# Kernel optimization log

Measured on AMD Instinct MI355X. Metric: run time of the kernel, lower is better.

## Reference

```python
import jax, jax.numpy as jnp
import numpy as np
from jax import lax

# Model dims (match init_kwargs / Mamba2 defaults)
B = 8; C_IN = 512; C_OUT = 512; H = 32; W = 32; L = H * W
D_STATE = 64; D_CONV = 4; EXPAND = 2; HEADDIM = 64
D_INNER = EXPAND * C_IN            # 1024
NHEADS = D_INNER // HEADDIM        # 16
D_XBC = D_INNER + 2 * D_STATE      # 1152 (ngroups=1)
D_IN_PROJ = 2 * D_INNER + 2 * D_STATE + NHEADS
EPS = 1e-5


def setup_inputs() -> dict:
    key = jax.random.key(0)
    ks = jax.random.split(key, 16)
    x = jax.random.normal(ks[0], (B, C_IN, H, W), jnp.float32)
    ln_w = jnp.ones((C_IN,), jnp.float32)
    ln_b = jnp.zeros((C_IN,), jnp.float32)
    in_proj_w = jax.random.normal(ks[1], (D_IN_PROJ, C_IN), jnp.float32) * 0.02
    conv1d_w = jax.random.normal(ks[2], (D_XBC, D_CONV), jnp.float32) * 0.2
    conv1d_b = jax.random.normal(ks[3], (D_XBC,), jnp.float32) * 0.02
    dt0 = jax.random.uniform(ks[4], (NHEADS,), jnp.float32, 1e-3, 0.1)
    dt_bias = jnp.log(jnp.expm1(dt0))  # inverse softplus init
    A_log = jnp.log(jax.random.uniform(ks[5], (NHEADS,), jnp.float32, 1.0, 16.0))
    D = jax.random.normal(ks[6], (NHEADS,), jnp.float32)
    rms_w = jnp.ones((D_INNER,), jnp.float32)
    out_proj_w = jax.random.normal(ks[7], (C_IN, D_INNER), jnp.float32) * 0.02
    conv2d_w = jax.random.normal(ks[8], (C_OUT, C_IN), jnp.float32) * 0.04
    conv2d_b = jnp.zeros((C_OUT,), jnp.float32)
    bn_g = jnp.ones((C_OUT,), jnp.float32)
    bn_b = jnp.zeros((C_OUT,), jnp.float32)
    bn_mean = jnp.zeros((C_OUT,), jnp.float32)
    bn_var = jnp.ones((C_OUT,), jnp.float32)
    return dict(x=x, ln_w=ln_w, ln_b=ln_b, in_proj_w=in_proj_w, conv1d_w=conv1d_w,
                conv1d_b=conv1d_b, dt_bias=dt_bias, A_log=A_log, D=D, rms_w=rms_w,
                out_proj_w=out_proj_w, conv2d_w=conv2d_w, conv2d_b=conv2d_b,
                bn_g=bn_g, bn_b=bn_b, bn_mean=bn_mean, bn_var=bn_var)


def reference(x, ln_w, ln_b, in_proj_w, conv1d_w, conv1d_b, dt_bias, A_log, D,
              rms_w, out_proj_w, conv2d_w, conv2d_b, bn_g, bn_b, bn_mean, bn_var):
    Bb, C, Hh, Ww = x.shape
    Ltok = Hh * Ww
    # tokens: (B, L, C)
    t = x.reshape(Bb, C, Ltok).transpose(0, 2, 1)
    # LayerNorm over channel dim
    mu = jnp.mean(t, -1, keepdims=True)
    var = jnp.mean(jnp.square(t - mu), -1, keepdims=True)
    xn = (t - mu) * lax.rsqrt(var + EPS) * ln_w + ln_b
    # Mamba2 in_proj -> [z, xBC, dt]
    zxbcdt = jnp.einsum('blc,dc->bld', xn, in_proj_w)
    z = zxbcdt[..., :D_INNER]
    xBC = zxbcdt[..., D_INNER:D_INNER + D_XBC]
    dt = zxbcdt[..., D_INNER + D_XBC:]                       # (B, L, nheads)
    # causal depthwise conv1d + silu
    conv = lax.conv_general_dilated(xBC.transpose(0, 2, 1), conv1d_w[:, None, :],
                                    window_strides=(1,), padding=[(D_CONV - 1, 0)],
                                    feature_group_count=D_XBC)
    xBC = jax.nn.silu(conv.transpose(0, 2, 1) + conv1d_b)
    xh = xBC[..., :D_INNER].reshape(Bb, Ltok, NHEADS, HEADDIM)
    Bm = xBC[..., D_INNER:D_INNER + D_STATE]                 # (B, L, d_state)
    Cm = xBC[..., D_INNER + D_STATE:]
    dt = jax.nn.softplus(dt + dt_bias)
    A = -jnp.exp(A_log)                                      # (nheads,)
    # selective scan (SSD recurrence), state h: (B, nheads, headdim, d_state)
    def step(h, inp):
        xt, dtt, Bt, Ct = inp
        dA = jnp.exp(dtt * A)                                # (B, nheads)
        h = h * dA[..., None, None] + jnp.einsum('bh,bhp,bs->bhps', dtt, xt, Bt)
        y = jnp.einsum('bhps,bs->bhp', h, Ct)
        return h, y
    h0 = jnp.zeros((Bb, NHEADS, HEADDIM, D_STATE), x.dtype)
    xs = (xh.transpose(1, 0, 2, 3), dt.transpose(1, 0, 2),
          Bm.transpose(1, 0, 2), Cm.transpose(1, 0, 2))
    _, ys = lax.scan(step, h0, xs)
    y = ys.transpose(1, 0, 2, 3) + D[None, None, :, None] * xh
    y = y.reshape(Bb, Ltok, D_INNER)
    # gated RMSNorm
    y = y * jax.nn.silu(z)
    y = y * lax.rsqrt(jnp.mean(y * y, -1, keepdims=True) + EPS) * rms_w
    out = jnp.einsum('bld,cd->blc', y, out_proj_w)
    img = out.transpose(0, 2, 1).reshape(Bb, C, Hh, Ww)
    # 1x1 conv + BN (inference) + ReLU
    c = jnp.einsum('bchw,oc->bohw', img, conv2d_w) + conv2d_b[None, :, None, None]
    c = (c - bn_mean[None, :, None, None]) * lax.rsqrt(bn_var + EPS)[None, :, None, None]
    c = c * bn_g[None, :, None, None] + bn_b[None, :, None, None]
    return jax.nn.relu(c)
```

## Files before the change

### kernel.cpp

```cpp
#include <hip/hip_runtime.h>
#include <hip/hip_bf16.h>

#define NB 8
#define LL 1024
#define CIN 512
#define DIN 1024
#define DXBC 1152
#define DPROJ 2192
#define NPADW 2304
#define NHH 16
#define HDD 64
#define DST 64
#define NCHUNK 16
#define QCH 64
#define XBCS 1024
#define CTT 8
#define DTB 16

typedef unsigned short u16;
typedef unsigned int u32;
typedef __bf16 bf16x8 __attribute__((ext_vector_type(8)));
typedef float f32x4 __attribute__((ext_vector_type(4)));
typedef u16 u16x8 __attribute__((ext_vector_type(8)));

__device__ __forceinline__ float bf2f(u16 u) {
    u32 x = ((u32)u) << 16; float f; __builtin_memcpy(&f, &x, 4); return f;
}
__device__ __forceinline__ u16 f2bf(float f) {
    u32 x; __builtin_memcpy(&x, &f, 4);
    u32 r = x + 0x7fff + ((x >> 16) & 1);
    return (u16)(r >> 16);
}

__device__ __forceinline__ void gload16(const u16* g, u16* l) {
    __builtin_amdgcn_global_load_lds((__attribute__((address_space(1))) void*)(g),
                                     (__attribute__((address_space(3))) void*)(l), 16, 0, 0);
}

__device__ __forceinline__ int swz(int row, int cb) {
    return row * 64 + ((cb ^ ((row & 7) << 4)) >> 1);
}

__global__ void f2bf_kernel(const float* __restrict__ s, u16* __restrict__ d, int n) {
    int i = blockIdx.x * 256 + threadIdx.x;
    if (i < n) d[i] = f2bf(s[i]);
}
__global__ void f2bf_pad(const float* __restrict__ s, u16* __restrict__ d, int nsrc, int ndst) {
    int i = blockIdx.x * 256 + threadIdx.x;
    if (i < ndst) d[i] = (i < nsrc) ? f2bf(s[i]) : (u16)0;
}
__global__ __launch_bounds__(256) void woutT_conv(const float* __restrict__ s,
                                                  const float* __restrict__ rw,
                                                  u16* __restrict__ dt) {
    __shared__ float tile[64][65];
    int bc = blockIdx.x & 7, bd = blockIdx.x >> 3;
    int c0 = bc * 64, d0 = bd * 64;
    int t = threadIdx.x;
    int r4 = t >> 6, cc = t & 63;
#pragma unroll
    for (int rr = 0; rr < 16; ++rr) {
        int row = r4 * 16 + rr;
        tile[row][cc] = s[(size_t)(c0 + row) * DIN + d0 + cc];
    }
    __syncthreads();
#pragma unroll
    for (int rr = 0; rr < 16; ++rr) {
        int row = r4 * 16 + rr;
        dt[(size_t)(d0 + row) * CIN + c0 + cc] = f2bf(tile[cc][row] * rw[d0 + row]);
    }
}
__global__ void bn_prep(const float* __restrict__ cb, const float* __restrict__ g,
                        const float* __restrict__ bb, const float* __restrict__ mean,
                        const float* __restrict__ var, float* __restrict__ scale,
                        float* __restrict__ shift) {
    int i = blockIdx.x * 256 + threadIdx.x;
    if (i < CIN) {
        float rs = rsqrtf(var[i] + 1e-5f);
        float sc = g[i] * rs;
        scale[i] = sc;
        shift[i] = (cb[i] - mean[i]) * sc + bb[i];
    }
}

__global__ __launch_bounds__(256) void ln_kernel(const float* __restrict__ x,
                                                 const float* __restrict__ lw,
                                                 const float* __restrict__ lb,
                                                 u16* __restrict__ xn) {
    __shared__ u16 tile[CIN * 33];
    __shared__ float psum[8][32], psq[8][32], muA[32], rsA[32];
    int bid = blockIdx.x;
    int b = bid >> 5, hw0 = (bid & 31) * 32;
    int t = threadIdx.x;
    int hw = t & 31, cg = t >> 5;
    const float* xb = x + (size_t)b * CIN * LL + hw0 + hw;
    float s = 0.f, sq = 0.f;
    for (int r = 0; r < CIN / 8; ++r) {
        int c = r * 8 + cg;
        float v = xb[(size_t)c * LL];
        s += v; sq += v * v;
        tile[c * 33 + hw] = f2bf(v);
    }
    psum[cg][hw] = s; psq[cg][hw] = sq;
    __syncthreads();
    if (t < 32) {
        float ss = 0.f, qq = 0.f;
        for (int g = 0; g < 8; ++g) { ss += psum[g][t]; qq += psq[g][t]; }
        float mu = ss * (1.f / CIN);
        float var = qq * (1.f / CIN) - mu * mu;
        muA[t] = mu; rsA[t] = rsqrtf(var + 1e-5f);
    }
    __syncthreads();
    for (int r = 0; r < 64; ++r) {
        int idx = r * 256 + t;
        int c = idx & (CIN - 1);
        int hh = idx >> 9;
        float v = (bf2f(tile[c * 33 + hh]) - muA[hh]) * rsA[hh] * lw[c] + lb[c];
        xn[((size_t)(b * LL + hw0 + hh)) * CIN + c] = f2bf(v);
    }
}

template <int EPI>
__global__ __launch_bounds__(256) void gemm_bt(const u16* __restrict__ A, const u16* __restrict__ Bw,
                                               void* __restrict__ Cout, int M, int N, int K, int ldc,
                                               int nx,
                                               const float* __restrict__ scale,
                                               const float* __restrict__ shift,
                                               const float* __restrict__ rsc) {
    __shared__ u16 As[2][128 * 64], Bs[2][128 * 64];
    int t = threadIdx.x;
    int lane = t & 63, wave = t >> 6;
    int nblk = gridDim.x;
    int qq = nblk >> 3, rm = nblk & 7;
    int xcd = blockIdx.x & 7, idx = blockIdx.x >> 3;
    int swzb = (xcd < rm ? xcd * (qq + 1) : rm * (qq + 1) + (xcd - rm) * qq) + idx;
    int m0 = (swzb / nx) * 128, n0 = (swzb % nx) * 128;
    int wr = wave >> 1, wc = wave & 1;
    f32x4 acc[4][4];
    for (int m = 0; m < 4; ++m)
        for (int n = 0; n < 4; ++n)
            for (int q = 0; q < 4; ++q) acc[m][n][q] = 0.f;

    const u16* Arow = A + (size_t)m0 * K;
    const u16* Brow = Bw + (size_t)n0 * K;
    int s4 = lane >> 4;
    int rr = lane & 15;

    auto STAGE = [&](int buf, int k0) {
#pragma unroll
        for (int j = 0; j < 4; ++j) {
            int e = j * 256 + t;
            int r = e >> 3, sr = e & 7;
            int src = (sr ^ (r & 7)) * 8;
            gload16(Arow + (size_t)r * K + k0 + src, &As[buf][e * 8]);
            gload16(Brow + (size_t)r * K + k0 + src, &Bs[buf][e * 8]);
        }
    };

    STAGE(0, 0);
    int NK = K >> 6, cur = 0;
    for (int kt = 0; kt < NK; ++kt) {
        if (kt + 1 < NK) {
            STAGE(cur ^ 1, (kt + 1) << 6);
            asm volatile("s_waitcnt vmcnt(8)" ::: "memory");
        } else {
            asm volatile("s_waitcnt vmcnt(0)" ::: "memory");
        }
        __builtin_amdgcn_s_barrier();
        __builtin_amdgcn_sched_barrier(0);
#pragma unroll
        for (int kk = 0; kk < 2; ++kk) {
            bf16x8 af[4], bfr[4];
#pragma unroll
            for (int m = 0; m < 4; ++m) {
                int row = wr * 64 + m * 16 + rr;
                int ss = (kk * 4 + s4) ^ (row & 7);
                af[m] = *(const bf16x8*)&As[cur][row * 64 + ss * 8];
            }
#pragma unroll
            for (int n = 0; n < 4; ++n) {
                int row = wc * 64 + n * 16 + rr;
                int ss = (kk * 4 + s4) ^ (row & 7);
                bfr[n] = *(const bf16x8*)&Bs[cur][row * 64 + ss * 8];
            }
#pragma unroll
            for (int m = 0; m < 4; ++m)
#pragma unroll
                for (int n = 0; n < 4; ++n)
                    acc[m][n] = __builtin_amdgcn_mfma_f32_16x16x32_bf16(af[m], bfr[n], acc[m][n], 0, 0, 0);
        }
        __builtin_amdgcn_s_barrier();
        cur ^= 1;
    }
    int fq = lane >> 4, fr = lane & 15;
#pragma unroll
    for (int m = 0; m < 4; ++m) {
#pragma unroll
        for (int n = 0; n < 4; ++n) {
            int col = n0 + wc * 64 + n * 16 + fr;
#pragma unroll
            for (int q = 0; q < 4; ++q) {
                int row = m0 + wr * 64 + m * 16 + fq * 4 + q;
                float v = acc[m][n][q];
                if (EPI == 0) {
                    ((u16*)Cout)[(size_t)row * ldc + col] = f2bf(v);
                } else {
                    v = v * rsc[col];
                    v = v * scale[row] + shift[row];
                    v = v > 0.f ? v : 0.f;
                    ((float*)Cout)[((size_t)(col >> 10)) * (CIN * LL) + (size_t)row * LL + (col & 1023)] = v;
                }
            }
        }
    }
}

__global__ __launch_bounds__(288) void conv1d_fused(const u16* __restrict__ zx,
                                                    const float* __restrict__ w,
                                                    const float* __restrict__ bias,
                                                    u16* __restrict__ xbc,
                                                    float* __restrict__ Bc, float* __restrict__ Cc) {
    int bid = blockIdx.x;
    int b = bid >> 7;
    int l0 = (bid & 127) * CTT;
    int t = threadIdx.x;
    bool isX = t < 256;
    int ch = isX ? t * 4 : 1024 + (t - 256) * 4;

    float4 wv0 = *(const float4*)&w[(ch + 0) * 4];
    float4 wv1 = *(const float4*)&w[(ch + 1) * 4];
    float4 wv2 = *(const float4*)&w[(ch + 2) * 4];
    float4 wv3 = *(const float4*)&w[(ch + 3) * 4];
    float4 bv = *(const float4*)&bias[ch];

    ushort4 xin[CTT + 3];
    const u16* src = zx + (size_t)(b * LL + l0 - 3) * NPADW + DIN + ch;
#pragma unroll
    for (int i = 0; i < CTT + 3; ++i) {
        ushort4 v = {0, 0, 0, 0};
        if (l0 + i - 3 >= 0) v = *(const ushort4*)(src + (size_t)i * NPADW);
        xin[i] = v;
    }
#pragma unroll
    for (int i = 0; i < CTT; ++i) {
        int tok = b * LL + l0 + i;
        float a0 = bv.x + bf2f(xin[i].x) * wv0.x + bf2f(xin[i + 1].x) * wv0.y +
                   bf2f(xin[i + 2].x) * wv0.z + bf2f(xin[i + 3].x) * wv0.w;
        float a1 = bv.y + bf2f(xin[i].y) * wv1.x + bf2f(xin[i + 1].y) * wv1.y +
                   bf2f(xin[i + 2].y) * wv1.z + bf2f(xin[i + 3].y) * wv1.w;
        float a2 = bv.z + bf2f(xin[i].z) * wv2.x + bf2f(xin[i + 1].z) * wv2.y +
                   bf2f(xin[i + 2].z) * wv2.z + bf2f(xin[i + 3].z) * wv2.w;
        float a3 = bv.w + bf2f(xin[i].w) * wv3.x + bf2f(xin[i + 1].w) * wv3.y +
                   bf2f(xin[i + 2].w) * wv3.z + bf2f(xin[i + 3].w) * wv3.w;
        float s0 = a0 / (1.f + __expf(-a0));
        float s1 = a1 / (1.f + __expf(-a1));
        float s2 = a2 / (1.f + __expf(-a2));
        float s3 = a3 / (1.f + __expf(-a3));
        if (isX) {
            ushort4 o;
            o.x = f2bf(s0); o.y = f2bf(s1); o.z = f2bf(s2); o.w = f2bf(s3);
            *(ushort4*)&xbc[(size_t)tok * XBCS + ch] = o;
        } else {
            int s = ch - 1024;
            float4 o4; o4.x = s0; o4.y = s1; o4.z = s2; o4.w = s3;
            if (s < DST) *(float4*)&Bc[(size_t)tok * DST + s] = o4;
            else         *(float4*)&Cc[(size_t)tok * DST + (s - DST)] = o4;
        }
    }
}

__global__ __launch_bounds__(256) void dt_gemv(const u16* __restrict__ xn,
                                               const float* __restrict__ wproj,
                                               const float* __restrict__ dt_bias,
                                               const float* __restrict__ A_log,
                                               float2* __restrict__ dtda) {
    int t = threadIdx.x;
    int h = t >> 4, part = t & 15;
    int tok0 = blockIdx.x * DTB;
    const float* wr = wproj + (size_t)(DIN + DXBC + h) * CIN + part * 32;
    float4 w[8];
#pragma unroll
    for (int i = 0; i < 8; ++i) w[i] = *(const float4*)&wr[i * 4];
    const float* wf = (const float*)w;
    float dtb = dt_bias[h];
    float An = -__expf(A_log[h]);
#pragma unroll
    for (int tl = 0; tl < DTB; ++tl) {
        int tok = tok0 + tl;
        const u16* xr = xn + (size_t)tok * CIN + part * 32;
        u16x8 xv0 = *(const u16x8*)&xr[0];
        u16x8 xv1 = *(const u16x8*)&xr[8];
        u16x8 xv2 = *(const u16x8*)&xr[16];
        u16x8 xv3 = *(const u16x8*)&xr[24];
        float s = 0.f;
#pragma unroll
        for (int i = 0; i < 8; ++i) s += bf2f(xv0[i]) * wf[i];
#pragma unroll
        for (int i = 0; i < 8; ++i) s += bf2f(xv1[i]) * wf[8 + i];
#pragma unroll
        for (int i = 0; i < 8; ++i) s += bf2f(xv2[i]) * wf[16 + i];
#pragma unroll
        for (int i = 0; i < 8; ++i) s += bf2f(xv3[i]) * wf[24 + i];
        s += __shfl_xor(s, 1, 64);
        s += __shfl_xor(s, 2, 64);
        s += __shfl_xor(s, 4, 64);
        s += __shfl_xor(s, 8, 64);
        if (part == 0) {
            float si = s + dtb;
            float dtv = si > 15.f ? si : __logf(1.f + __expf(si));
            float2 dd; dd.x = dtv; dd.y = dtv * An;
            dtda[(size_t)tok * NHH + h] = dd;
        }
    }
}

__global__ __launch_bounds__(256) void ssd_chunk(const float* __restrict__ Bcb,
                                                 const float* __restrict__ Ccb,
                                                 const u16* __restrict__ xbc,
                                                 const float2* __restrict__ dtda,
                                                 u16* __restrict__ yi,
                                                 u16* __restrict__ DHb,
                                                 float* __restrict__ ESA,
                                                 float* __restrict__ DC) {
    __shared__ u16 Bt[4096], Ct[4096], XT[4096], BTt[4096], Gt[4096];
    __shared__ float Sar[64], dtvA[64], wA[64];
    int tau = blockIdx.x;
    int b = tau >> 8, h = (tau >> 4) & 15, c = tau & 15;
    int t0g = b * LL + c * QCH;
    int t = threadIdx.x, lane = t & 63, wave = t >> 6;
    int row = t >> 2, q = t & 3;

    {
        const float* bp = Bcb + (size_t)(t0g + row) * DST + q * 16;
        const float* cp = Ccb + (size_t)(t0g + row) * DST + q * 16;
#pragma unroll
        for (int half = 0; half < 2; ++half) {
            float4 v0 = *(const float4*)(bp + half * 8);
            float4 v1 = *(const float4*)(bp + half * 8 + 4);
            u16x8 o;
            o[0] = f2bf(v0.x); o[1] = f2bf(v0.y); o[2] = f2bf(v0.z); o[3] = f2bf(v0.w);
            o[4] = f2bf(v1.x); o[5] = f2bf(v1.y); o[6] = f2bf(v1.z); o[7] = f2bf(v1.w);
            *(u16x8*)&Bt[swz(row, q * 32 + half * 16)] = o;
            float4 c0 = *(const float4*)(cp + half * 8);
            float4 c1 = *(const float4*)(cp + half * 8 + 4);
            u16x8 oc;
            oc[0] = f2bf(c0.x); oc[1] = f2bf(c0.y); oc[2] = f2bf(c0.z); oc[3] = f2bf(c0.w);
            oc[4] = f2bf(c1.x); oc[5] = f2bf(c1.y); oc[6] = f2bf(c1.z); oc[7] = f2bf(c1.w);
            *(u16x8*)&Ct[swz(row, q * 32 + half * 16)] = oc;
        }
        const u16* xp = xbc + (size_t)(t0g + row) * XBCS + h * HDD + q * 16;
        u16x8 x0 = *(const u16x8*)xp;
        u16x8 x1 = *(const u16x8*)(xp + 8);
#pragma unroll
        for (int e = 0; e < 8; ++e) XT[swz(q * 16 + e, row * 2)] = x0[e];
#pragma unroll
        for (int e = 0; e < 8; ++e) XT[swz(q * 16 + 8 + e, row * 2)] = x1[e];
    }
    if (t < 64) {
        float2 dd = dtda[(size_t)(t0g + t) * NHH + h];
        float s = dd.y;
#pragma unroll
        for (int off = 1; off < 64; off <<= 1) {
            float u = __shfl_up(s, off, 64);
            if (t >= off) s += u;
        }
        float SQ = __shfl(s, 63, 64);
        Sar[t] = s; dtvA[t] = dd.x;
        wA[t] = __expf(SQ - s) * dd.x;
        ESA[(size_t)tau * 64 + t] = __expf(s);
        if (t == 0) DC[tau] = __expf(SQ);
    }
    __syncthreads();

    int R = wave >> 1, Cq = wave & 1, rr = lane & 15, sg = lane >> 4;
    f32x4 g[2][2];
#pragma unroll
    for (int mi = 0; mi < 2; ++mi)
#pragma unroll
        for (int ni = 0; ni < 2; ++ni)
#pragma unroll
            for (int r = 0; r < 4; ++r) g[mi][ni][r] = 0.f;
#pragma unroll
    for (int kt = 0; kt < 2; ++kt) {
        int cb = kt * 64 + sg * 16;
        bf16x8 a0 = *(const bf16x8*)&Ct[swz(R * 32 + rr, cb)];
        bf16x8 a1 = *(const bf16x8*)&Ct[swz(R * 32 + 16 + rr, cb)];
        bf16x8 b0 = *(const bf16x8*)&Bt[swz(Cq * 32 + rr, cb)];
        bf16x8 b1 = *(const bf16x8*)&Bt[swz(Cq * 32 + 16 + rr, cb)];
        g[0][0] = __builtin_amdgcn_mfma_f32_16x16x32_bf16(a0, b0, g[0][0], 0, 0, 0);
        g[0][1] = __builtin_amdgcn_mfma_f32_16x16x32_bf16(a0, b1, g[0][1], 0, 0, 0);
        g[1][0] = __builtin_amdgcn_mfma_f32_16x16x32_bf16(a1, b0, g[1][0], 0, 0, 0);
        g[1][1] = __builtin_amdgcn_mfma_f32_16x16x32_bf16(a1, b1, g[1][1], 0, 0, 0);
    }
#pragma unroll
    for (int mi = 0; mi < 2; ++mi)
#pragma unroll
        for (int ni = 0; ni < 2; ++ni)
#pragma unroll
            for (int r = 0; r < 4; ++r) {
                int i = R * 32 + mi * 16 + sg * 4 + r;
                int j = Cq * 32 + ni * 16 + rr;
                float v = (i >= j) ? g[mi][ni][r] * __expf(Sar[i] - Sar[j]) * dtvA[j] : 0.f;
                Gt[swz(i, j * 2)] = f2bf(v);
            }
#pragma unroll
    for (int half = 0; half < 2; ++half) {
        u16x8 bv = *(const u16x8*)&Bt[swz(row, q * 32 + half * 16)];
#pragma unroll
        for (int e = 0; e < 8; ++e)
            BTt[swz(q * 16 + half * 8 + e, row * 2)] = f2bf(bf2f(bv[e]) * wA[row]);
    }
    __syncthreads();

    f32x4 y[2][2], dh[2][2];
#pragma unroll
    for (int mi = 0; mi < 2; ++mi)
#pragma unroll
        for (int ni = 0; ni < 2; ++ni)
#pragma unroll
            for (int r = 0; r < 4; ++r) { y[mi][ni][r] = 0.f; dh[mi][ni][r] = 0.f; }
#pragma unroll
    for (int kt = 0; kt < 2; ++kt) {
        int cb = kt * 64 + sg * 16;
        bf16x8 xb0 = *(const bf16x8*)&XT[swz(Cq * 32 + rr, cb)];
        bf16x8 xb1 = *(const bf16x8*)&XT[swz(Cq * 32 + 16 + rr, cb)];
        bf16x8 ga0 = *(const bf16x8*)&Gt[swz(R * 32 + rr, cb)];
        bf16x8 ga1 = *(const bf16x8*)&Gt[swz(R * 32 + 16 + rr, cb)];
        bf16x8 ba0 = *(const bf16x8*)&BTt[swz(R * 32 + rr, cb)];
        bf16x8 ba1 = *(const bf16x8*)&BTt[swz(R * 32 + 16 + rr, cb)];
        y[0][0] = __builtin_amdgcn_mfma_f32_16x16x32_bf16(ga0, xb0, y[0][0], 0, 0, 0);
        y[0][1] = __builtin_amdgcn_mfma_f32_16x16x32_bf16(ga0, xb1, y[0][1], 0, 0, 0);
        y[1][0] = __builtin_amdgcn_mfma_f32_16x16x32_bf16(ga1, xb0, y[1][0], 0, 0, 0);
        y[1][1] = __builtin_amdgcn_mfma_f32_16x16x32_bf16(ga1, xb1, y[1][1], 0, 0, 0);
        dh[0][0] = __builtin_amdgcn_mfma_f32_16x16x32_bf16(ba0, xb0, dh[0][0], 0, 0, 0);
        dh[0][1] = __builtin_amdgcn_mfma_f32_16x16x32_bf16(ba0, xb1, dh[0][1], 0, 0, 0);
        dh[1][0] = __builtin_amdgcn_mfma_f32_16x16x32_bf16(ba1, xb0, dh[1][0], 0, 0, 0);
        dh[1][1] = __builtin_amdgcn_mfma_f32_16x16x32_bf16(ba1, xb1, dh[1][1], 0, 0, 0);
    }
#pragma unroll
    for (int mi = 0; mi < 2; ++mi)
#pragma unroll
        for (int ni = 0; ni < 2; ++ni)
#pragma unroll
            for (int r = 0; r < 4; ++r) {
                int i = R * 32 + mi * 16 + sg * 4 + r;
                int p = Cq * 32 + ni * 16 + rr;
                yi[(size_t)(t0g + i) * DIN + h * HDD + p] = f2bf(y[mi][ni][r]);
                DHb[(size_t)tau * 4096 + i * 64 + p] = f2bf(dh[mi][ni][r]);
            }
}

__global__ __launch_bounds__(256) void ssd_carry(const u16* __restrict__ DHb,
                                                 const float* __restrict__ DC,
                                                 u16* __restrict__ HPREV) {
    int bid = blockIdx.x;
    int bh = bid >> 1, ph = bid & 1;
    int t = threadIdx.x;
    int s = t >> 2, p0 = ph * 32 + (t & 3) * 8;
    size_t base = (size_t)bh * NCHUNK * 4096 + s * 64 + p0;
    float Hv[8] = {0.f, 0.f, 0.f, 0.f, 0.f, 0.f, 0.f, 0.f};
    for (int c = 0; c < NCHUNK; ++c) {
        size_t off = base + (size_t)c * 4096;
        u16x8 hp;
#pragma unroll
        for (int e = 0; e < 8; ++e) hp[e] = f2bf(Hv[e]);
        *(u16x8*)&HPREV[off] = hp;
        float d = DC[bh * NCHUNK + c];
        u16x8 dv = *(const u16x8*)&DHb[off];
#pragma unroll
        for (int e = 0; e < 8; ++e) Hv[e] = d * Hv[e] + bf2f(dv[e]);
    }
}

__global__ __launch_bounds__(256) void ssd_final(const float* __restrict__ Ccb,
                                                 const float* __restrict__ ESA,
                                                 const u16* __restrict__ HPREV,
                                                 const u16* __restrict__ xbc,
                                                 const u16* __restrict__ zx,
                                                 const float* __restrict__ Dp,
                                                 u16* __restrict__ yi,
                                                 float* __restrict__ PS) {
    __shared__ u16 C2t[4096], HT[4096];
    __shared__ float smem_ps[2][64];
    int tau = blockIdx.x;
    int b = tau >> 8, h = (tau >> 4) & 15, c = tau & 15;
    int t0g = b * LL + c * QCH;
    int t = threadIdx.x, lane = t & 63, wave = t >> 6;
    int row = t >> 2, q = t & 3;
    {
        float esa = ESA[(size_t)tau * 64 + row];
        const float* cp = Ccb + (size_t)(t0g + row) * DST + q * 16;
#pragma unroll
        for (int half = 0; half < 2; ++half) {
            float4 c0 = *(const float4*)(cp + half * 8);
            float4 c1 = *(const float4*)(cp + half * 8 + 4);
            u16x8 oc;
            oc[0] = f2bf(c0.x * esa); oc[1] = f2bf(c0.y * esa);
            oc[2] = f2bf(c0.z * esa); oc[3] = f2bf(c0.w * esa);
            oc[4] = f2bf(c1.x * esa); oc[5] = f2bf(c1.y * esa);
            oc[6] = f2bf(c1.z * esa); oc[7] = f2bf(c1.w * esa);
            *(u16x8*)&C2t[swz(row, q * 32 + half * 16)] = oc;
            u16x8 hv = *(const u16x8*)&HPREV[(size_t)tau * 4096 + row * 64 + q * 16 + half * 8];
#pragma unroll
            for (int e = 0; e < 8; ++e) HT[swz(q * 16 + half * 8 + e, row * 2)] = hv[e];
        }
    }
    __syncthreads();
    int R = wave >> 1, Cq = wave & 1, rr = lane & 15, sg = lane >> 4;
    float Dh = Dp[h];
    f32x4 acc[2][2];
#pragma unroll
    for (int mi = 0; mi < 2; ++mi)
#pragma unroll
        for (int ni = 0; ni < 2; ++ni)
#pragma unroll
            for (int r = 0; r < 4; ++r) {
                int i = R * 32 + mi * 16 + sg * 4 + r;
                int p = Cq * 32 + ni * 16 + rr;
                acc[mi][ni][r] = bf2f(yi[(size_t)(t0g + i) * DIN + h * HDD + p]);
            }
#pragma unroll
    for (int kt = 0; kt < 2; ++kt) {
        int cb = kt * 64 + sg * 16;
        bf16x8 a0 = *(const bf16x8*)&C2t[swz(R * 32 + rr, cb)];
        bf16x8 a1 = *(const bf16x8*)&C2t[swz(R * 32 + 16 + rr, cb)];
        bf16x8 b0 = *(const bf16x8*)&HT[swz(Cq * 32 + rr, cb)];
        bf16x8 b1 = *(const bf16x8*)&HT[swz(Cq * 32 + 16 + rr, cb)];
        acc[0][0] = __builtin_amdgcn_mfma_f32_16x16x32_bf16(a0, b0, acc[0][0], 0, 0, 0);
        acc[0][1] = __builtin_amdgcn_mfma_f32_16x16x32_bf16(a0, b1, acc[0][1], 0, 0, 0);
        acc[1][0] = __builtin_amdgcn_mfma_f32_16x16x32_bf16(a1, b0, acc[1][0], 0, 0, 0);
        acc[1][1] = __builtin_amdgcn_mfma_f32_16x16x32_bf16(a1, b1, acc[1][1], 0, 0, 0);
    }
    float ps[2][4];
#pragma unroll
    for (int mi = 0; mi < 2; ++mi)
#pragma unroll
        for (int r = 0; r < 4; ++r) ps[mi][r] = 0.f;
#pragma unroll
    for (int mi = 0; mi < 2; ++mi)
#pragma unroll
        for (int ni = 0; ni < 2; ++ni)
#pragma unroll
            for (int r = 0; r < 4; ++r) {
                int i = R * 32 + mi * 16 + sg * 4 + r;
                int p = Cq * 32 + ni * 16 + rr;
                size_t tok = t0g + i;
                int col = h * HDD + p;
                float xf = bf2f(xbc[tok * XBCS + col]);
                float zf = bf2f(zx[tok * NPADW + col]);
                float yo = (acc[mi][ni][r] + Dh * xf) * (zf / (1.f + __expf(-zf)));
                yi[tok * DIN + col] = f2bf(yo);
                ps[mi][r] += yo * yo;
            }
#pragma unroll
    for (int mi = 0; mi < 2; ++mi)
#pragma unroll
        for (int r = 0; r < 4; ++r) {
            float s2 = ps[mi][r];
            s2 += __shfl_xor(s2, 1, 64);
            s2 += __shfl_xor(s2, 2, 64);
            s2 += __shfl_xor(s2, 4, 64);
            s2 += __shfl_xor(s2, 8, 64);
            if (rr == 0) smem_ps[Cq][R * 32 + mi * 16 + sg * 4 + r] = s2;
        }
    __syncthreads();
    if (t < 64) PS[(size_t)tau * 64 + t] = smem_ps[0][t] + smem_ps[1][t];
}

__global__ __launch_bounds__(256) void rs_from_ps(const float* __restrict__ PS,
                                                  float* __restrict__ RS) {
    int tok = blockIdx.x * 256 + threadIdx.x;
    int b = tok >> 10, rem = tok & 1023;
    int c = rem >> 6, i = rem & 63;
    float s = 0.f;
#pragma unroll
    for (int h = 0; h < NHH; ++h)
        s += PS[(size_t)(((b << 4) + h) * 16 + c) * 64 + i];
    RS[tok] = rsqrtf(s * (1.f / DIN) + 1e-5f);
}

extern "C" void kernel_launch(void* const* d_in, const int* in_sizes, int n_in,
                              void* d_out, int out_size, void* d_ws, size_t ws_size,
                              hipStream_t stream) {
    const float* x         = (const float*)d_in[0];
    const float* ln_w      = (const float*)d_in[1];
    const float* ln_b      = (const float*)d_in[2];
    const float* in_proj_w = (const float*)d_in[3];
    const float* conv1d_w  = (const float*)d_in[4];
    const float* conv1d_b  = (const float*)d_in[5];
    const float* dt_bias   = (const float*)d_in[6];
    const float* A_log     = (const float*)d_in[7];
    const float* Dp        = (const float*)d_in[8];
    const float* rms_w     = (const float*)d_in[9];
    const float* out_proj_w= (const float*)d_in[10];
    const float* conv2d_w  = (const float*)d_in[11];
    const float* conv2d_b  = (const float*)d_in[12];
    const float* bn_g      = (const float*)d_in[13];
    const float* bn_b      = (const float*)d_in[14];
    const float* bn_mean   = (const float*)d_in[15];
    const float* bn_var    = (const float*)d_in[16];

    const int TOK = NB * LL;
    const int NTAU = NB * NHH * NCHUNK;
    char* ws = (char*)d_ws;
    size_t off = 0;
    auto alloc = [&](size_t bytes) {
        void* p = ws + off;
        off += (bytes + 255) & ~(size_t)255;
        return p;
    };
    u16*   Win   = (u16*)alloc((size_t)NPADW * CIN * 2);
    u16*   WoutT = (u16*)alloc((size_t)DIN * CIN * 2);
    u16*   Wc2   = (u16*)alloc((size_t)CIN * CIN * 2);
    u16*   WCMB  = (u16*)alloc((size_t)CIN * DIN * 2);
    u16*   XN    = (u16*)alloc((size_t)TOK * CIN * 2);
    u16*   ZX    = (u16*)alloc((size_t)TOK * NPADW * 2);
    u16*   XBC   = (u16*)alloc((size_t)TOK * XBCS * 2);
    float* Bcb   = (float*)alloc((size_t)TOK * DST * 4);
    float* Ccb   = (float*)alloc((size_t)TOK * DST * 4);
    float2* DTDA = (float2*)alloc((size_t)TOK * NHH * 8);
    u16*   YI    = (u16*)alloc((size_t)TOK * DIN * 2);
    u16*   DHb   = (u16*)alloc((size_t)NTAU * 4096 * 2);
    u16*   HPREV = (u16*)alloc((size_t)NTAU * 4096 * 2);
    float* ESA   = (float*)alloc((size_t)NTAU * 64 * 4);
    float* PS    = (float*)alloc((size_t)NTAU * 64 * 4);
    float* DC    = (float*)alloc((size_t)NTAU * 4);
    float* RS    = (float*)alloc((size_t)TOK * 4);
    float* BNSC  = (float*)alloc(CIN * 4);
    float* BNSH  = (float*)alloc(CIN * 4);

    f2bf_pad<<<(NPADW * CIN + 255) / 256, 256, 0, stream>>>(in_proj_w, Win, DPROJ * CIN, NPADW * CIN);
    woutT_conv<<<128, 256, 0, stream>>>(out_proj_w, rms_w, WoutT);
    f2bf_kernel<<<(CIN * CIN + 255) / 256, 256, 0, stream>>>(conv2d_w, Wc2, CIN * CIN);
    bn_prep<<<2, 256, 0, stream>>>(conv2d_b, bn_g, bn_b, bn_mean, bn_var, BNSC, BNSH);
    gemm_bt<0><<<(CIN / 128) * (DIN / 128), 256, 0, stream>>>(Wc2, WoutT, WCMB, CIN, DIN, CIN, DIN,
                                                              DIN / 128, nullptr, nullptr, nullptr);

    ln_kernel<<<256, 256, 0, stream>>>(x, ln_w, ln_b, XN);

    gemm_bt<0><<<(TOK / 128) * (NPADW / 128), 256, 0, stream>>>(XN, Win, ZX, TOK, NPADW, CIN, NPADW,
                                                                NPADW / 128, nullptr, nullptr, nullptr);

    conv1d_fused<<<NB * (LL / CTT), 288, 0, stream>>>(ZX, conv1d_w, conv1d_b, XBC, Bcb, Ccb);
    dt_gemv<<<TOK / DTB, 256, 0, stream>>>(XN, in_proj_w, dt_bias, A_log, DTDA);

    ssd_chunk<<<NTAU, 256, 0, stream>>>(Bcb, Ccb, XBC, DTDA, YI, DHb, ESA, DC);
    ssd_carry<<<256, 256, 0, stream>>>(DHb, DC, HPREV);
    ssd_final<<<NTAU, 256, 0, stream>>>(Ccb, ESA, HPREV, XBC, ZX, Dp, YI, PS);

    rs_from_ps<<<TOK / 256, 256, 0, stream>>>(PS, RS);

    gemm_bt<1><<<(CIN / 128) * (TOK / 128), 256, 0, stream>>>(WCMB, YI, d_out, CIN, TOK, DIN, 0,
                                                              TOK / 128, BNSC, BNSH, RS);
}
```

Before: 161.5 us.

## Shrink GEMM N-tile to 64 and store B/C SSM inputs as bf16

The shared GEMM kernel now uses 128x64 output tiles instead of 128x128, doubling the block count for all three GEMM launches and halving per-wave accumulators, with the B-tile staging loop and wait count adjusted to match. Separately, conv1d writes the B and C state projections as bf16 instead of fp32, so ssd_chunk and ssd_final read half the bytes and skip the in-kernel fp32-to-bf16 conversion. The smaller tile gives more parallelism and occupancy but lowers arithmetic reuse per block and loads more A traffic.

```diff
diff --git a/kernel.cpp b/kernel.cpp
--- a/kernel.cpp
+++ b/kernel.cpp
@@ -126,18 +126,18 @@
                                                const float* __restrict__ scale,
                                                const float* __restrict__ shift,
                                                const float* __restrict__ rsc) {
-    __shared__ u16 As[2][128 * 64], Bs[2][128 * 64];
+    __shared__ u16 As[2][128 * 64], Bs[2][64 * 64];
     int t = threadIdx.x;
     int lane = t & 63, wave = t >> 6;
     int nblk = gridDim.x;
     int qq = nblk >> 3, rm = nblk & 7;
     int xcd = blockIdx.x & 7, idx = blockIdx.x >> 3;
     int swzb = (xcd < rm ? xcd * (qq + 1) : rm * (qq + 1) + (xcd - rm) * qq) + idx;
-    int m0 = (swzb / nx) * 128, n0 = (swzb % nx) * 128;
+    int m0 = (swzb / nx) * 128, n0 = (swzb % nx) * 64;
     int wr = wave >> 1, wc = wave & 1;
-    f32x4 acc[4][4];
+    f32x4 acc[4][2];
     for (int m = 0; m < 4; ++m)
-        for (int n = 0; n < 4; ++n)
+        for (int n = 0; n < 2; ++n)
             for (int q = 0; q < 4; ++q) acc[m][n][q] = 0.f;
 
     const u16* Arow = A + (size_t)m0 * K;
@@ -152,6 +152,12 @@
             int r = e >> 3, sr = e & 7;
             int src = (sr ^ (r & 7)) * 8;
             gload16(Arow + (size_t)r * K + k0 + src, &As[buf][e * 8]);
+        }
+#pragma unroll
+        for (int j = 0; j < 2; ++j) {
+            int e = j * 256 + t;
+            int r = e >> 3, sr = e & 7;
+            int src = (sr ^ (r & 7)) * 8;
             gload16(Brow + (size_t)r * K + k0 + src, &Bs[buf][e * 8]);
         }
     };
@@ -161,7 +167,7 @@
     for (int kt = 0; kt < NK; ++kt) {
         if (kt + 1 < NK) {
             STAGE(cur ^ 1, (kt + 1) << 6);
-            asm volatile("s_waitcnt vmcnt(8)" ::: "memory");
+            asm volatile("s_waitcnt vmcnt(6)" ::: "memory");
         } else {
             asm volatile("s_waitcnt vmcnt(0)" ::: "memory");
         }
@@ -169,7 +175,7 @@
         __builtin_amdgcn_sched_barrier(0);
 #pragma unroll
         for (int kk = 0; kk < 2; ++kk) {
-            bf16x8 af[4], bfr[4];
+            bf16x8 af[4], bfr[2];
 #pragma unroll
             for (int m = 0; m < 4; ++m) {
                 int row = wr * 64 + m * 16 + rr;
@@ -177,15 +183,15 @@
                 af[m] = *(const bf16x8*)&As[cur][row * 64 + ss * 8];
             }
 #pragma unroll
-            for (int n = 0; n < 4; ++n) {
-                int row = wc * 64 + n * 16 + rr;
+            for (int n = 0; n < 2; ++n) {
+                int row = wc * 32 + n * 16 + rr;
                 int ss = (kk * 4 + s4) ^ (row & 7);
                 bfr[n] = *(const bf16x8*)&Bs[cur][row * 64 + ss * 8];
             }
 #pragma unroll
             for (int m = 0; m < 4; ++m)
 #pragma unroll
-                for (int n = 0; n < 4; ++n)
+                for (int n = 0; n < 2; ++n)
                     acc[m][n] = __builtin_amdgcn_mfma_f32_16x16x32_bf16(af[m], bfr[n], acc[m][n], 0, 0, 0);
         }
         __builtin_amdgcn_s_barrier();
@@ -195,8 +201,8 @@
 #pragma unroll
     for (int m = 0; m < 4; ++m) {
 #pragma unroll
-        for (int n = 0; n < 4; ++n) {
-            int col = n0 + wc * 64 + n * 16 + fr;
+        for (int n = 0; n < 2; ++n) {
+            int col = n0 + wc * 32 + n * 16 + fr;
 #pragma unroll
             for (int q = 0; q < 4; ++q) {
                 int row = m0 + wr * 64 + m * 16 + fq * 4 + q;
@@ -218,7 +224,7 @@
                                                     const float* __restrict__ w,
                                                     const float* __restrict__ bias,
                                                     u16* __restrict__ xbc,
-                                                    float* __restrict__ Bc, float* __restrict__ Cc) {
+                                                    u16* __restrict__ Bc, u16* __restrict__ Cc) {
     int bid = blockIdx.x;
     int b = bid >> 7;
     int l0 = (bid & 127) * CTT;
@@ -255,15 +261,14 @@
         float s1 = a1 / (1.f + __expf(-a1));
         float s2 = a2 / (1.f + __expf(-a2));
         float s3 = a3 / (1.f + __expf(-a3));
+        ushort4 o;
+        o.x = f2bf(s0); o.y = f2bf(s1); o.z = f2bf(s2); o.w = f2bf(s3);
         if (isX) {
-            ushort4 o;
-            o.x = f2bf(s0); o.y = f2bf(s1); o.z = f2bf(s2); o.w = f2bf(s3);
             *(ushort4*)&xbc[(size_t)tok * XBCS + ch] = o;
         } else {
             int s = ch - 1024;
-            float4 o4; o4.x = s0; o4.y = s1; o4.z = s2; o4.w = s3;
-            if (s < DST) *(float4*)&Bc[(size_t)tok * DST + s] = o4;
-            else         *(float4*)&Cc[(size_t)tok * DST + (s - DST)] = o4;
+            if (s < DST) *(ushort4*)&Bc[(size_t)tok * DST + s] = o;
+            else         *(ushort4*)&Cc[(size_t)tok * DST + (s - DST)] = o;
         }
     }
 }
@@ -313,8 +318,8 @@
     }
 }
 
-__global__ __launch_bounds__(256) void ssd_chunk(const float* __restrict__ Bcb,
-                                                 const float* __restrict__ Ccb,
+__global__ __launch_bounds__(256) void ssd_chunk(const u16* __restrict__ Bcb,
+                                                 const u16* __restrict__ Ccb,
                                                  const u16* __restrict__ xbc,
                                                  const float2* __restrict__ dtda,
                                                  u16* __restrict__ yi,
@@ -330,23 +335,16 @@
     int row = t >> 2, q = t & 3;
 
     {
-        const float* bp = Bcb + (size_t)(t0g + row) * DST + q * 16;
-        const float* cp = Ccb + (size_t)(t0g + row) * DST + q * 16;
-#pragma unroll
-        for (int half = 0; half < 2; ++half) {
-            float4 v0 = *(const float4*)(bp + half * 8);
-            float4 v1 = *(const float4*)(bp + half * 8 + 4);
-            u16x8 o;
-            o[0] = f2bf(v0.x); o[1] = f2bf(v0.y); o[2] = f2bf(v0.z); o[3] = f2bf(v0.w);
-            o[4] = f2bf(v1.x); o[5] = f2bf(v1.y); o[6] = f2bf(v1.z); o[7] = f2bf(v1.w);
-            *(u16x8*)&Bt[swz(row, q * 32 + half * 16)] = o;
-            float4 c0 = *(const float4*)(cp + half * 8);
-            float4 c1 = *(const float4*)(cp + half * 8 + 4);
-            u16x8 oc;
-            oc[0] = f2bf(c0.x); oc[1] = f2bf(c0.y); oc[2] = f2bf(c0.z); oc[3] = f2bf(c0.w);
-            oc[4] = f2bf(c1.x); oc[5] = f2bf(c1.y); oc[6] = f2bf(c1.z); oc[7] = f2bf(c1.w);
-            *(u16x8*)&Ct[swz(row, q * 32 + half * 16)] = oc;
-        }
+        const u16* bp = Bcb + (size_t)(t0g + row) * DST + q * 16;
+        const u16* cp = Ccb + (size_t)(t0g + row) * DST + q * 16;
+        u16x8 b0v = *(const u16x8*)bp;
+        u16x8 b1v = *(const u16x8*)(bp + 8);
+        *(u16x8*)&Bt[swz(row, q * 32)] = b0v;
+        *(u16x8*)&Bt[swz(row, q * 32 + 16)] = b1v;
+        u16x8 c0v = *(const u16x8*)cp;
+        u16x8 c1v = *(const u16x8*)(cp + 8);
+        *(u16x8*)&Ct[swz(row, q * 32)] = c0v;
+        *(u16x8*)&Ct[swz(row, q * 32 + 16)] = c1v;
         const u16* xp = xbc + (size_t)(t0g + row) * XBCS + h * HDD + q * 16;
         u16x8 x0 = *(const u16x8*)xp;
         u16x8 x1 = *(const u16x8*)(xp + 8);
@@ -471,7 +469,7 @@
     }
 }
 
-__global__ __launch_bounds__(256) void ssd_final(const float* __restrict__ Ccb,
+__global__ __launch_bounds__(256) void ssd_final(const u16* __restrict__ Ccb,
                                                  const float* __restrict__ ESA,
                                                  const u16* __restrict__ HPREV,
                                                  const u16* __restrict__ xbc,
@@ -488,16 +486,13 @@
     int row = t >> 2, q = t & 3;
     {
         float esa = ESA[(size_t)tau * 64 + row];
-        const float* cp = Ccb + (size_t)(t0g + row) * DST + q * 16;
+        const u16* cp = Ccb + (size_t)(t0g + row) * DST + q * 16;
 #pragma unroll
         for (int half = 0; half < 2; ++half) {
-            float4 c0 = *(const float4*)(cp + half * 8);
-            float4 c1 = *(const float4*)(cp + half * 8 + 4);
+            u16x8 cv = *(const u16x8*)(cp + half * 8);
             u16x8 oc;
-            oc[0] = f2bf(c0.x * esa); oc[1] = f2bf(c0.y * esa);
-            oc[2] = f2bf(c0.z * esa); oc[3] = f2bf(c0.w * esa);
-            oc[4] = f2bf(c1.x * esa); oc[5] = f2bf(c1.y * esa);
-            oc[6] = f2bf(c1.z * esa); oc[7] = f2bf(c1.w * esa);
+#pragma unroll
+            for (int e = 0; e < 8; ++e) oc[e] = f2bf(bf2f(cv[e]) * esa);
             *(u16x8*)&C2t[swz(row, q * 32 + half * 16)] = oc;
             u16x8 hv = *(const u16x8*)&HPREV[(size_t)tau * 4096 + row * 64 + q * 16 + half * 8];
 #pragma unroll
@@ -615,8 +610,8 @@
     u16*   XN    = (u16*)alloc((size_t)TOK * CIN * 2);
     u16*   ZX    = (u16*)alloc((size_t)TOK * NPADW * 2);
     u16*   XBC   = (u16*)alloc((size_t)TOK * XBCS * 2);
-    float* Bcb   = (float*)alloc((size_t)TOK * DST * 4);
-    float* Ccb   = (float*)alloc((size_t)TOK * DST * 4);
+    u16*   Bcb   = (u16*)alloc((size_t)TOK * DST * 2);
+    u16*   Ccb   = (u16*)alloc((size_t)TOK * DST * 2);
     float2* DTDA = (float2*)alloc((size_t)TOK * NHH * 8);
     u16*   YI    = (u16*)alloc((size_t)TOK * DIN * 2);
     u16*   DHb   = (u16*)alloc((size_t)NTAU * 4096 * 2);
@@ -632,13 +627,13 @@
     woutT_conv<<<128, 256, 0, stream>>>(out_proj_w, rms_w, WoutT);
     f2bf_kernel<<<(CIN * CIN + 255) / 256, 256, 0, stream>>>(conv2d_w, Wc2, CIN * CIN);
     bn_prep<<<2, 256, 0, stream>>>(conv2d_b, bn_g, bn_b, bn_mean, bn_var, BNSC, BNSH);
-    gemm_bt<0><<<(CIN / 128) * (DIN / 128), 256, 0, stream>>>(Wc2, WoutT, WCMB, CIN, DIN, CIN, DIN,
-                                                              DIN / 128, nullptr, nullptr, nullptr);
+    gemm_bt<0><<<(CIN / 128) * (DIN / 64), 256, 0, stream>>>(Wc2, WoutT, WCMB, CIN, DIN, CIN, DIN,
+                                                             DIN / 64, nullptr, nullptr, nullptr);
 
     ln_kernel<<<256, 256, 0, stream>>>(x, ln_w, ln_b, XN);
 
-    gemm_bt<0><<<(TOK / 128) * (NPADW / 128), 256, 0, stream>>>(XN, Win, ZX, TOK, NPADW, CIN, NPADW,
-                                                                NPADW / 128, nullptr, nullptr, nullptr);
+    gemm_bt<0><<<(TOK / 128) * (NPADW / 64), 256, 0, stream>>>(XN, Win, ZX, TOK, NPADW, CIN, NPADW,
+                                                               NPADW / 64, nullptr, nullptr, nullptr);
 
     conv1d_fused<<<NB * (LL / CTT), 288, 0, stream>>>(ZX, conv1d_w, conv1d_b, XBC, Bcb, Ccb);
     dt_gemv<<<TOK / DTB, 256, 0, stream>>>(XN, in_proj_w, dt_bias, A_log, DTDA);
@@ -649,6 +644,6 @@
 
     rs_from_ps<<<TOK / 256, 256, 0, stream>>>(PS, RS);
 
-    gemm_bt<1><<<(CIN / 128) * (TOK / 128), 256, 0, stream>>>(WCMB, YI, d_out, CIN, TOK, DIN, 0,
-                                                              TOK / 128, BNSC, BNSH, RS);
-}
+    gemm_bt<1><<<(CIN / 128) * (TOK / 64), 256, 0, stream>>>(WCMB, YI, d_out, CIN, TOK, DIN, 0,
+                                                             TOK / 64, BNSC, BNSH, RS);
+}
```

Result: faster. 152.4 us (-5.6%).
